# Kernel tuning notes

Measured on AMD Instinct MI355X. Metric: run time of the kernel, lower is better.

The kernel has to match this reference:

```python
import jax, jax.numpy as jnp
import numpy as np


def setup_inputs() -> dict:
    key = jax.random.key(0)
    ks = jax.random.split(key, 8)
    B, N, E_PER, M = 8, 50000, 1000000, 2048  # graphs, nodes/graph, edges/graph, decision neurons
    BN, E = B * N, B * E_PER
    x = jax.random.normal(ks[0], (BN, 1), dtype=jnp.float32)
    edge_weight = jax.random.uniform(ks[1], (E,), minval=0.0, maxval=10.0, dtype=jnp.float32)
    # within-graph edges with PyG-style batch offsets
    offs = jnp.repeat(jnp.arange(B, dtype=jnp.int32) * N, E_PER)
    src = jax.random.randint(ks[2], (E,), 0, N, dtype=jnp.int32) + offs
    dst = jax.random.randint(ks[3], (E,), 0, N, dtype=jnp.int32) + offs
    # indices where decision_making_vector == 1 (static for jit)
    dm_indices = jnp.sort(jax.random.randint(ks[4], (M,), 0, N, dtype=jnp.int32))
    fc_w = jax.random.normal(ks[5], (1, 1), dtype=jnp.float32)
    fc_b = jax.random.normal(ks[6], (1,), dtype=jnp.float32)
    return {"x": x, "edge_weight": edge_weight, "src": src, "dst": dst,
            "dm_indices": dm_indices, "fc_w": fc_w, "fc_b": fc_b,
            "batch_size": 8, "num_passes": 3}


def reference(x, edge_weight, src, dst, dm_indices, fc_w, fc_b, batch_size, num_passes):
    # log1p edge transform
    ew = jnp.log1p(edge_weight)  # [E]
    BN = x.shape[0]
    N = BN // batch_size
    h = x  # [BN, 1]
    # TrainableEdgeConv: num_passes rounds of scatter-add message passing + per-graph L2 norm over nodes
    for _ in range(num_passes):
        msgs = h[src] * ew[:, None]                      # [E, 1] gather + scale
        h = jax.ops.segment_sum(msgs, dst, num_segments=BN)  # scatter-add to dst
        hb = h.reshape(batch_size, N, -1)
        hb = hb / jnp.linalg.norm(hb, axis=1, keepdims=True)  # x / x.norm(dim=1)
        h = hb.reshape(BN, -1)
    # decision_making_mask: select decision neurons
    v = h.reshape(batch_size, N, -1)[:, dm_indices, 0]  # [B, M]
    # normalize_non_zero: per-graph mean/std over nonzero entries (unbiased std, like scatter_std)
    mask = v != 0
    cnt = mask.sum(axis=1, keepdims=True).astype(v.dtype)
    mean = jnp.where(mask, v, 0.0).sum(axis=1, keepdims=True) / cnt
    var = jnp.where(mask, (v - mean) ** 2, 0.0).sum(axis=1, keepdims=True) / jnp.maximum(cnt - 1.0, 1.0)
    std = jnp.sqrt(var) + 1e-5
    v = jnp.where(mask, (v - mean) / std, v)
    # mean pool over decision neurons, Linear(1,1), relu, squeeze -> [B]
    pooled = v.mean(axis=1)  # [B]
    out = pooled * fc_w[0, 0] + fc_b[0]
    return jax.nn.relu(out)
```

## Files before the change

### kernel.cpp

```cpp
#include <hip/hip_runtime.h>
#include <math.h>

#define GB    8
#define GN    50000
#define EPG   1000000
#define EDGES (GB*EPG)
#define NP    3

#define BW     4096
#define NBUCK  13
#define NBINS  (GB*NBUCK)
#define CAP    89088
#define CPB    10
#define STRIPE 4000
#define NQ     (STRIPE/4)
#define NBLKH  (EDGES/STRIPE)
#define BPG    (EPG/STRIPE)
#define SRCMASK 0x7FFFFu


__global__ void z_k(int* __restrict__ gcur, float* __restrict__ nsq) {
  int t = threadIdx.x;
  if (t < NBINS) gcur[t] = 0;
  if (t < GB) nsq[t] = 0.f;
}

__global__ __launch_bounds__(256) void fscatter_k(
    const int* __restrict__ src, const int* __restrict__ dst,
    const float* __restrict__ ew, int* __restrict__ gcur,
    uint2* __restrict__ recs) {
  __shared__ int lh[NBINS];
  __shared__ int lb[NBINS];
  if (threadIdx.x < NBINS) lh[threadIdx.x] = 0;
  __syncthreads();
  int blk = blockIdx.x;
  int s0 = blk * STRIPE;
  int g = blk / BPG;
  int base = g * GN, gb = g * NBUCK;
  const int4* d4 = (const int4*)(dst + s0);
  const int4* s4 = (const int4*)(src + s0);
  const float4* w4 = (const float4*)(ew + s0);

  int rk[16];
#pragma unroll
  for (int u = 0; u < 4; ++u) {
    int q = threadIdx.x + 256 * u;
    if (q < NQ) {
      int4 d = d4[q];
      rk[4 * u + 0] = atomicAdd(&lh[gb + ((d.x - base) >> 12)], 1);
      rk[4 * u + 1] = atomicAdd(&lh[gb + ((d.y - base) >> 12)], 1);
      rk[4 * u + 2] = atomicAdd(&lh[gb + ((d.z - base) >> 12)], 1);
      rk[4 * u + 3] = atomicAdd(&lh[gb + ((d.w - base) >> 12)], 1);
    }
  }
  __syncthreads();
  if (threadIdx.x < NBINS) {
    int c = lh[threadIdx.x];
    lb[threadIdx.x] = c ? atomicAdd(&gcur[threadIdx.x], c) : 0;
  }
  __syncthreads();
#pragma unroll
  for (int u = 0; u < 4; ++u) {
    int q = threadIdx.x + 256 * u;
    if (q < NQ) {
      int4 d = d4[q]; int4 s = s4[q]; float4 w = w4[q];
      int dv[4] = {d.x, d.y, d.z, d.w};
      int sv[4] = {s.x, s.y, s.z, s.w};
      float wv[4] = {w.x, w.y, w.z, w.w};
#pragma unroll
      for (int k = 0; k < 4; ++k) {
        int dl = dv[k] - base;
        int bin = gb + (dl >> 12);
        int r = dl & (BW - 1);
        size_t pos = (size_t)bin * CAP + lb[bin] + rk[4 * u + k];
        recs[pos] = make_uint2(((unsigned)r << 19) | (unsigned)sv[k],
                               __float_as_uint(log1pf(wv[k])));
      }
    }
  }
}

__global__ __launch_bounds__(256) void accum_k(
    const uint2* __restrict__ recs, const int* __restrict__ cnt,
    const float* __restrict__ hin, float* __restrict__ partials) {
  __shared__ float acc[BW];
  int c = blockIdx.x;
  int bin = blockIdx.y;
  float4 z = {0.f, 0.f, 0.f, 0.f};
  float4* a4 = (float4*)acc;
  for (int i = threadIdx.x; i < BW / 4; i += 256) a4[i] = z;
  int len = cnt[bin];
  int chunk = ((len + CPB - 1) / CPB + 1) & ~1;
  int lo = c * chunk;
  int hi = lo + chunk;
  if (lo > len) lo = len;
  if (hi > len) hi = len;
  const uint2* rb = recs + (size_t)bin * CAP;
  __syncthreads();
  int rem = hi - lo;
  if (rem < 0) rem = 0;
  int np = rem >> 1;
  const uint4* rp = (const uint4*)(rb + lo);
  int p = threadIdx.x;
  for (; p + 256 < np; p += 512) {
    uint4 r0 = rp[p];
    uint4 r1 = rp[p + 256];
    float a0 = hin[r0.x & SRCMASK] * __uint_as_float(r0.y);
    float a1 = hin[r0.z & SRCMASK] * __uint_as_float(r0.w);
    float a2 = hin[r1.x & SRCMASK] * __uint_as_float(r1.y);
    float a3 = hin[r1.z & SRCMASK] * __uint_as_float(r1.w);
    atomicAdd(&acc[r0.x >> 19], a0);
    atomicAdd(&acc[r0.z >> 19], a1);
    atomicAdd(&acc[r1.x >> 19], a2);
    atomicAdd(&acc[r1.z >> 19], a3);
  }
  if (p < np) {
    uint4 r0 = rp[p];
    atomicAdd(&acc[r0.x >> 19], hin[r0.x & SRCMASK] * __uint_as_float(r0.y));
    atomicAdd(&acc[r0.z >> 19], hin[r0.z & SRCMASK] * __uint_as_float(r0.w));
  }
  if ((rem & 1) && threadIdx.x == 0) {
    uint2 a = rb[hi - 1];
    atomicAdd(&acc[a.x >> 19], hin[a.x & SRCMASK] * __uint_as_float(a.y));
  }
  __syncthreads();
  float4* po = (float4*)(partials + ((size_t)bin * CPB + c) * BW);
  for (int i = threadIdx.x; i < BW / 4; i += 256) po[i] = a4[i];
}

__global__ void reduce_k(const float* __restrict__ partials,
                         float* __restrict__ hout, float* __restrict__ nsq) {
  __shared__ float sm[GB];
  if (threadIdx.x < GB) sm[threadIdx.x] = 0.f;
  __syncthreads();
  int n4 = blockIdx.x * 256 + threadIdx.x;
  if (n4 < (GB * GN) / 4) {
    int n = n4 * 4;
    int g = n / GN;
    int dl = n - g * GN;
    int bucket = dl >> 12;
    int slot = dl & (BW - 1);
    const float4* p = (const float4*)(partials +
        ((size_t)(g * NBUCK + bucket) * CPB) * BW + slot);
    float4 s = {0.f, 0.f, 0.f, 0.f};
#pragma unroll
    for (int c = 0; c < CPB; ++c) {
      float4 t = p[c * (BW / 4)];
      s.x += t.x; s.y += t.y; s.z += t.z; s.w += t.w;
    }
    ((float4*)hout)[n4] = s;
    if (nsq) atomicAdd(&sm[g], s.x * s.x + s.y * s.y + s.z * s.z + s.w * s.w);
  }
  __syncthreads();
  if (nsq && threadIdx.x < GB && sm[threadIdx.x] != 0.f)
    unsafeAtomicAdd(&nsq[threadIdx.x], sm[threadIdx.x]);
}


__global__ void init_k(const float* __restrict__ x, float* __restrict__ h_cur,
                       float* __restrict__ h_next, float* __restrict__ norms,
                       int BN, int n_norms) {
  int i = blockIdx.x * blockDim.x + threadIdx.x;
  int stride = gridDim.x * blockDim.x;
  for (int j = i; j < BN; j += stride) { h_cur[j] = x[j]; h_next[j] = 0.f; }
  if (i < n_norms) norms[i] = 0.f;
}

__global__ void edge_k(const int* __restrict__ src, const int* __restrict__ dst,
                       const float* __restrict__ ew, const float* __restrict__ h_in,
                       float* __restrict__ h_out, int E4, int E) {
  int i = blockIdx.x * blockDim.x + threadIdx.x;
  int stride = gridDim.x * blockDim.x;
  const int4* s4 = (const int4*)src;
  const int4* d4 = (const int4*)dst;
  const float4* w4 = (const float4*)ew;
  for (int j = i; j < E4; j += stride) {
    int4 s = s4[j]; int4 d = d4[j]; float4 w = w4[j];
    unsafeAtomicAdd(&h_out[d.x], h_in[s.x] * log1pf(w.x));
    unsafeAtomicAdd(&h_out[d.y], h_in[s.y] * log1pf(w.y));
    unsafeAtomicAdd(&h_out[d.z], h_in[s.z] * log1pf(w.z));
    unsafeAtomicAdd(&h_out[d.w], h_in[s.w] * log1pf(w.w));
  }
  for (int j = E4 * 4 + i; j < E; j += stride)
    unsafeAtomicAdd(&h_out[dst[j]], h_in[src[j]] * log1pf(ew[j]));
}

__global__ void norm_k(const float* __restrict__ h, float* __restrict__ norms, int N) {
  int g = blockIdx.y;
  const float* hg = h + (size_t)g * N;
  float s = 0.f;
  for (int j = blockIdx.x * blockDim.x + threadIdx.x; j < N; j += gridDim.x * blockDim.x) {
    float v = hg[j]; s += v * v;
  }
  __shared__ float sm[4];
  for (int o = 32; o > 0; o >>= 1) s += __shfl_down(s, o, 64);
  if ((threadIdx.x & 63) == 0) sm[threadIdx.x >> 6] = s;
  __syncthreads();
  if (threadIdx.x == 0) {
    float t = 0.f;
    for (int w = 0; w < (int)(blockDim.x >> 6); ++w) t += sm[w];
    unsafeAtomicAdd(&norms[g], t);
  }
}

__global__ void scale_k(const float* __restrict__ norms, float* __restrict__ h_next,
                        float* __restrict__ h_cur, int N) {
  int g = blockIdx.y;
  float inv = 1.0f / sqrtf(norms[g]);
  size_t off = (size_t)g * N;
  for (int j = blockIdx.x * blockDim.x + threadIdx.x; j < N; j += gridDim.x * blockDim.x) {
    h_cur[off + j] = h_next[off + j] * inv;
    h_next[off + j] = 0.f;
  }
}

__device__ __forceinline__ float blk_red(float t, float* sm, int nw) {
  for (int o = 32; o > 0; o >>= 1) t += __shfl_down(t, o, 64);
  if ((threadIdx.x & 63) == 0) sm[threadIdx.x >> 6] = t;
  __syncthreads();
  float r = 0.f;
  for (int w = 0; w < nw; ++w) r += sm[w];
  __syncthreads();
  return r;
}

__global__ void final_k(const float* __restrict__ h, const float* __restrict__ nsq,
                        const int* __restrict__ dm,
                        const float* __restrict__ fc_w, const float* __restrict__ fc_b,
                        float* __restrict__ out, int N, int M) {
  extern __shared__ float v[];
  __shared__ float sm[16];
  int b = blockIdx.x;
  int nw = blockDim.x >> 6;
  float inv = nsq ? 1.0f / sqrtf(nsq[b]) : 1.0f;
  const float* hb = h + (size_t)b * N;
  for (int m = threadIdx.x; m < M; m += blockDim.x) v[m] = hb[dm[m]] * inv;
  __syncthreads();

  float cnt = 0.f, sum = 0.f;
  for (int m = threadIdx.x; m < M; m += blockDim.x) {
    float xv = v[m];
    if (xv != 0.f) { cnt += 1.f; sum += xv; }
  }
  float totalSum = blk_red(sum, sm, nw);
  float totalCnt = blk_red(cnt, sm, nw);
  float mean = totalCnt > 0.f ? totalSum / totalCnt : 0.f;

  float ssq = 0.f;
  for (int m = threadIdx.x; m < M; m += blockDim.x) {
    float xv = v[m];
    if (xv != 0.f) { float d = xv - mean; ssq += d * d; }
  }
  float totalSsq = blk_red(ssq, sm, nw);

  float denom = totalCnt - 1.f;
  if (denom < 1.f) denom = 1.f;
  float stdv = sqrtf(totalSsq / denom) + 1e-5f;

  float ps = 0.f;
  for (int m = threadIdx.x; m < M; m += blockDim.x) {
    float xv = v[m];
    if (xv != 0.f) ps += (xv - mean) / stdv;
  }
  float pooled = blk_red(ps, sm, nw) / (float)M;
  if (threadIdx.x == 0) {
    float o = pooled * fc_w[0] + fc_b[0];
    out[b] = o > 0.f ? o : 0.f;
  }
}

extern "C" void kernel_launch(void* const* d_in, const int* in_sizes, int n_in,
                              void* d_out, int out_size, void* d_ws, size_t ws_size,
                              hipStream_t stream) {
  const float* x    = (const float*)d_in[0];
  const float* ew   = (const float*)d_in[1];
  const int*   src  = (const int*)d_in[2];
  const int*   dst  = (const int*)d_in[3];
  const int*   dm   = (const int*)d_in[4];
  const float* fc_w = (const float*)d_in[5];
  const float* fc_b = (const float*)d_in[6];

  const int BN = in_sizes[0];
  const int E  = in_sizes[1];
  const int M  = in_sizes[4];
  const int N  = BN / GB;

  const bool shapes_ok = (BN == GB * GN) && (E == EDGES);

  const size_t recs_b  = (size_t)NBINS * CAP * 8;
  const size_t part_b  = (size_t)NBINS * CPB * BW * 4;
  const size_t buf_b   = (size_t)BN * 4;
  const size_t misc_b  = 4096;
  const size_t REQ = recs_b + part_b + 2 * buf_b + misc_b;

  if (shapes_ok && ws_size >= REQ) {
    uint2* recs     = (uint2*)d_ws;
    float* partials = (float*)((char*)d_ws + recs_b);
    float* bufA     = (float*)((char*)partials + part_b);
    float* bufB     = (float*)((char*)bufA + buf_b);
    char*  misc     = (char*)bufB + buf_b;
    int*   gcur     = (int*)misc;
    float* nsq      = (float*)(gcur + NBINS + 8);

    z_k<<<1, 128, 0, stream>>>(gcur, nsq);
    fscatter_k<<<NBLKH, 256, 0, stream>>>(src, dst, ew, gcur, recs);

    int rgrid = (BN / 4 + 255) / 256;
    dim3 agrid(CPB, NBINS);
    accum_k<<<agrid, 256, 0, stream>>>(recs, gcur, x, partials);
    reduce_k<<<rgrid, 256, 0, stream>>>(partials, bufA, nullptr);
    accum_k<<<agrid, 256, 0, stream>>>(recs, gcur, bufA, partials);
    reduce_k<<<rgrid, 256, 0, stream>>>(partials, bufB, nullptr);
    accum_k<<<agrid, 256, 0, stream>>>(recs, gcur, bufB, partials);
    reduce_k<<<rgrid, 256, 0, stream>>>(partials, bufA, nsq);

    final_k<<<GB, 512, M * sizeof(float), stream>>>(bufA, nsq, dm, fc_w, fc_b,
                                                    (float*)d_out, N, M);
    return;
  }

  float* h_cur  = (float*)d_ws;
  float* h_next = h_cur + BN;
  float* norms  = h_next + BN;
  const int threads = 256;
  init_k<<<(BN + threads - 1) / threads, threads, 0, stream>>>(x, h_cur, h_next,
                                                               norms, BN, NP * GB);
  int E4 = E / 4;
  int edgeBlocks = (E4 + threads - 1) / threads;
  dim3 ngrid((N + threads * 8 - 1) / (threads * 8), GB);
  for (int p = 0; p < NP; ++p) {
    edge_k<<<edgeBlocks, threads, 0, stream>>>(src, dst, ew, h_cur, h_next, E4, E);
    norm_k<<<ngrid, threads, 0, stream>>>(h_next, norms + p * GB, N);
    scale_k<<<ngrid, threads, 0, stream>>>(norms + p * GB, h_next, h_cur, N);
  }
  final_k<<<GB, 256, M * sizeof(float), stream>>>(h_cur, nullptr, dm, fc_w, fc_b,
                                                  (float*)d_out, N, M);
}
```

Measured before the change: 334.6 us.

## Bin edges by source and destination bucket to stage h in LDS

Edges are now binned into a 2D grid of (source bucket, destination bucket) per graph, using an added counting pass and a prefix-scan so records are packed compactly rather than held in fixed-capacity bins. Each accumulation block loads its 4096-entry source slice of h into shared memory, which replaces random global gathers with LDS reads. The cost is an extra full read of src and dst in the count pass and a scan kernel. Blocks are now split by source bucket instead of fixed chunks, so per-block work is less even, and the reduce step sums 13 partials per destination instead of 10.

```diff
diff --git a/kernel.cpp b/kernel.cpp
--- a/kernel.cpp
+++ b/kernel.cpp
@@ -9,34 +9,93 @@
 
 #define BW     4096
 #define NBUCK  13
-#define NBINS  (GB*NBUCK)
-#define CAP    89088
-#define CPB    10
+#define LBINS  (NBUCK*NBUCK)
+#define NB2    (GB*LBINS)
 #define STRIPE 4000
 #define NQ     (STRIPE/4)
 #define NBLKH  (EDGES/STRIPE)
 #define BPG    (EPG/STRIPE)
-#define SRCMASK 0x7FFFFu
-
-
-__global__ void z_k(int* __restrict__ gcur, float* __restrict__ nsq) {
-  int t = threadIdx.x;
-  if (t < NBINS) gcur[t] = 0;
-  if (t < GB) nsq[t] = 0.f;
-}
-
-__global__ __launch_bounds__(256) void fscatter_k(
+#define SCHUNK 6
+
+
+__global__ void z_k(int* __restrict__ gcur, int* __restrict__ cnt,
+                    float* __restrict__ nsq) {
+  for (int i = threadIdx.x; i < NB2; i += 256) { gcur[i] = 0; cnt[i] = 0; }
+  if (threadIdx.x < GB) nsq[threadIdx.x] = 0.f;
+}
+
+__global__ __launch_bounds__(256) void count_k(
     const int* __restrict__ src, const int* __restrict__ dst,
-    const float* __restrict__ ew, int* __restrict__ gcur,
-    uint2* __restrict__ recs) {
-  __shared__ int lh[NBINS];
-  __shared__ int lb[NBINS];
-  if (threadIdx.x < NBINS) lh[threadIdx.x] = 0;
+    int* __restrict__ cnt) {
+  __shared__ int lh[LBINS];
+  for (int i = threadIdx.x; i < LBINS; i += 256) lh[i] = 0;
   __syncthreads();
   int blk = blockIdx.x;
   int s0 = blk * STRIPE;
   int g = blk / BPG;
-  int base = g * GN, gb = g * NBUCK;
+  int base = g * GN;
+  const int4* d4 = (const int4*)(dst + s0);
+  const int4* s4 = (const int4*)(src + s0);
+#pragma unroll
+  for (int u = 0; u < 4; ++u) {
+    int q = threadIdx.x + 256 * u;
+    if (q < NQ) {
+      int4 d = d4[q]; int4 s = s4[q];
+      atomicAdd(&lh[((s.x - base) >> 12) * NBUCK + ((d.x - base) >> 12)], 1);
+      atomicAdd(&lh[((s.y - base) >> 12) * NBUCK + ((d.y - base) >> 12)], 1);
+      atomicAdd(&lh[((s.z - base) >> 12) * NBUCK + ((d.z - base) >> 12)], 1);
+      atomicAdd(&lh[((s.w - base) >> 12) * NBUCK + ((d.w - base) >> 12)], 1);
+    }
+  }
+  __syncthreads();
+  int gb = g * LBINS;
+  for (int i = threadIdx.x; i < LBINS; i += 256) {
+    int c = lh[i];
+    if (c) atomicAdd(&cnt[gb + i], c);
+  }
+}
+
+__global__ void scan_k(const int* __restrict__ cnt, int* __restrict__ basea) {
+  __shared__ int ps[256];
+  int t = threadIdx.x;
+  int loc[SCHUNK];
+  int s = 0;
+#pragma unroll
+  for (int k = 0; k < SCHUNK; ++k) {
+    int i = t * SCHUNK + k;
+    int a = (i < NB2) ? ((cnt[i] + 1) & ~1) : 0;
+    loc[k] = s;
+    s += a;
+  }
+  ps[t] = s;
+  __syncthreads();
+  for (int o = 1; o < 256; o <<= 1) {
+    int u = (t >= o) ? ps[t - o] : 0;
+    __syncthreads();
+    ps[t] += u;
+    __syncthreads();
+  }
+  int ex = t ? ps[t - 1] : 0;
+#pragma unroll
+  for (int k = 0; k < SCHUNK; ++k) {
+    int i = t * SCHUNK + k;
+    if (i < NB2) basea[i] = ex + loc[k];
+  }
+  if (t == 255) basea[NB2] = ps[255];
+}
+
+__global__ __launch_bounds__(256) void fscatter_k(
+    const int* __restrict__ src, const int* __restrict__ dst,
+    const float* __restrict__ ew, const int* __restrict__ basea,
+    int* __restrict__ gcur, uint2* __restrict__ recs) {
+  __shared__ int lh[LBINS];
+  __shared__ int lb[LBINS];
+  for (int i = threadIdx.x; i < LBINS; i += 256) lh[i] = 0;
+  __syncthreads();
+  int blk = blockIdx.x;
+  int s0 = blk * STRIPE;
+  int g = blk / BPG;
+  int base = g * GN, gb = g * LBINS;
   const int4* d4 = (const int4*)(dst + s0);
   const int4* s4 = (const int4*)(src + s0);
   const float4* w4 = (const float4*)(ew + s0);
@@ -46,17 +105,17 @@
   for (int u = 0; u < 4; ++u) {
     int q = threadIdx.x + 256 * u;
     if (q < NQ) {
-      int4 d = d4[q];
-      rk[4 * u + 0] = atomicAdd(&lh[gb + ((d.x - base) >> 12)], 1);
-      rk[4 * u + 1] = atomicAdd(&lh[gb + ((d.y - base) >> 12)], 1);
-      rk[4 * u + 2] = atomicAdd(&lh[gb + ((d.z - base) >> 12)], 1);
-      rk[4 * u + 3] = atomicAdd(&lh[gb + ((d.w - base) >> 12)], 1);
+      int4 d = d4[q]; int4 s = s4[q];
+      rk[4 * u + 0] = atomicAdd(&lh[((s.x - base) >> 12) * NBUCK + ((d.x - base) >> 12)], 1);
+      rk[4 * u + 1] = atomicAdd(&lh[((s.y - base) >> 12) * NBUCK + ((d.y - base) >> 12)], 1);
+      rk[4 * u + 2] = atomicAdd(&lh[((s.z - base) >> 12) * NBUCK + ((d.z - base) >> 12)], 1);
+      rk[4 * u + 3] = atomicAdd(&lh[((s.w - base) >> 12) * NBUCK + ((d.w - base) >> 12)], 1);
     }
   }
   __syncthreads();
-  if (threadIdx.x < NBINS) {
-    int c = lh[threadIdx.x];
-    lb[threadIdx.x] = c ? atomicAdd(&gcur[threadIdx.x], c) : 0;
+  for (int i = threadIdx.x; i < LBINS; i += 256) {
+    int c = lh[i];
+    lb[i] = (c ? atomicAdd(&gcur[gb + i], c) : 0) + basea[gb + i];
   }
   __syncthreads();
 #pragma unroll
@@ -70,10 +129,11 @@
 #pragma unroll
       for (int k = 0; k < 4; ++k) {
         int dl = dv[k] - base;
-        int bin = gb + (dl >> 12);
-        int r = dl & (BW - 1);
-        size_t pos = (size_t)bin * CAP + lb[bin] + rk[4 * u + k];
-        recs[pos] = make_uint2(((unsigned)r << 19) | (unsigned)sv[k],
+        int sl = sv[k] - base;
+        int l = (sl >> 12) * NBUCK + (dl >> 12);
+        int pos = lb[l] + rk[4 * u + k];
+        recs[pos] = make_uint2(((unsigned)(dl & (BW - 1)) << 12) |
+                               (unsigned)(sl & (BW - 1)),
                                __float_as_uint(log1pf(wv[k])));
       }
     }
@@ -81,50 +141,54 @@
 }
 
 __global__ __launch_bounds__(256) void accum_k(
-    const uint2* __restrict__ recs, const int* __restrict__ cnt,
-    const float* __restrict__ hin, float* __restrict__ partials) {
+    const uint2* __restrict__ recs, const int* __restrict__ basea,
+    const int* __restrict__ cnt, const float* __restrict__ hin,
+    float* __restrict__ partials) {
+  __shared__ float sh[BW];
   __shared__ float acc[BW];
-  int c = blockIdx.x;
-  int bin = blockIdx.y;
+  int sb = blockIdx.x;
+  int gdb = blockIdx.y;
+  int g = gdb / NBUCK, db = gdb - g * NBUCK;
+  int bin = g * LBINS + sb * NBUCK + db;
+
   float4 z = {0.f, 0.f, 0.f, 0.f};
   float4* a4 = (float4*)acc;
   for (int i = threadIdx.x; i < BW / 4; i += 256) a4[i] = z;
+  int sw = GN - sb * BW; if (sw > BW) sw = BW;
+  const float4* hp = (const float4*)(hin + (size_t)g * GN + (size_t)sb * BW);
+  float4* sp = (float4*)sh;
+  for (int i = threadIdx.x; i < sw / 4; i += 256) sp[i] = hp[i];
+
   int len = cnt[bin];
-  int chunk = ((len + CPB - 1) / CPB + 1) & ~1;
-  int lo = c * chunk;
-  int hi = lo + chunk;
-  if (lo > len) lo = len;
-  if (hi > len) hi = len;
-  const uint2* rb = recs + (size_t)bin * CAP;
-  __syncthreads();
-  int rem = hi - lo;
-  if (rem < 0) rem = 0;
-  int np = rem >> 1;
-  const uint4* rp = (const uint4*)(rb + lo);
+  const uint2* rb = recs + basea[bin];
+  __syncthreads();
+
+  int np = len >> 1;
+  const uint4* rp = (const uint4*)rb;
   int p = threadIdx.x;
   for (; p + 256 < np; p += 512) {
     uint4 r0 = rp[p];
     uint4 r1 = rp[p + 256];
-    float a0 = hin[r0.x & SRCMASK] * __uint_as_float(r0.y);
-    float a1 = hin[r0.z & SRCMASK] * __uint_as_float(r0.w);
-    float a2 = hin[r1.x & SRCMASK] * __uint_as_float(r1.y);
-    float a3 = hin[r1.z & SRCMASK] * __uint_as_float(r1.w);
-    atomicAdd(&acc[r0.x >> 19], a0);
-    atomicAdd(&acc[r0.z >> 19], a1);
-    atomicAdd(&acc[r1.x >> 19], a2);
-    atomicAdd(&acc[r1.z >> 19], a3);
+    float a0 = sh[r0.x & (BW - 1)] * __uint_as_float(r0.y);
+    float a1 = sh[r0.z & (BW - 1)] * __uint_as_float(r0.w);
+    float a2 = sh[r1.x & (BW - 1)] * __uint_as_float(r1.y);
+    float a3 = sh[r1.z & (BW - 1)] * __uint_as_float(r1.w);
+    atomicAdd(&acc[r0.x >> 12], a0);
+    atomicAdd(&acc[r0.z >> 12], a1);
+    atomicAdd(&acc[r1.x >> 12], a2);
+    atomicAdd(&acc[r1.z >> 12], a3);
   }
   if (p < np) {
     uint4 r0 = rp[p];
-    atomicAdd(&acc[r0.x >> 19], hin[r0.x & SRCMASK] * __uint_as_float(r0.y));
-    atomicAdd(&acc[r0.z >> 19], hin[r0.z & SRCMASK] * __uint_as_float(r0.w));
-  }
-  if ((rem & 1) && threadIdx.x == 0) {
-    uint2 a = rb[hi - 1];
-    atomicAdd(&acc[a.x >> 19], hin[a.x & SRCMASK] * __uint_as_float(a.y));
-  }
-  __syncthreads();
-  float4* po = (float4*)(partials + ((size_t)bin * CPB + c) * BW);
+    atomicAdd(&acc[r0.x >> 12], sh[r0.x & (BW - 1)] * __uint_as_float(r0.y));
+    atomicAdd(&acc[r0.z >> 12], sh[r0.z & (BW - 1)] * __uint_as_float(r0.w));
+  }
+  if ((len & 1) && threadIdx.x == 0) {
+    uint2 a = rb[len - 1];
+    atomicAdd(&acc[a.x >> 12], sh[a.x & (BW - 1)] * __uint_as_float(a.y));
+  }
+  __syncthreads();
+  float4* po = (float4*)(partials + ((size_t)gdb * NBUCK + sb) * BW);
   for (int i = threadIdx.x; i < BW / 4; i += 256) po[i] = a4[i];
 }
 
@@ -141,10 +205,10 @@
     int bucket = dl >> 12;
     int slot = dl & (BW - 1);
     const float4* p = (const float4*)(partials +
-        ((size_t)(g * NBUCK + bucket) * CPB) * BW + slot);
+        ((size_t)(g * NBUCK + bucket) * NBUCK) * BW + slot);
     float4 s = {0.f, 0.f, 0.f, 0.f};
 #pragma unroll
-    for (int c = 0; c < CPB; ++c) {
+    for (int c = 0; c < NBUCK; ++c) {
       float4 t = p[c * (BW / 4)];
       s.x += t.x; s.y += t.y; s.z += t.z; s.w += t.w;
     }
@@ -287,10 +351,10 @@
 
   const bool shapes_ok = (BN == GB * GN) && (E == EDGES);
 
-  const size_t recs_b  = (size_t)NBINS * CAP * 8;
-  const size_t part_b  = (size_t)NBINS * CPB * BW * 4;
-  const size_t buf_b   = (size_t)BN * 4;
-  const size_t misc_b  = 4096;
+  const size_t recs_b = (size_t)(EDGES + 4096) * 8;
+  const size_t part_b = (size_t)GB * NBUCK * NBUCK * BW * 4;
+  const size_t buf_b  = (size_t)BN * 4;
+  const size_t misc_b = 65536;
   const size_t REQ = recs_b + part_b + 2 * buf_b + misc_b;
 
   if (shapes_ok && ws_size >= REQ) {
@@ -300,18 +364,22 @@
     float* bufB     = (float*)((char*)bufA + buf_b);
     char*  misc     = (char*)bufB + buf_b;
     int*   gcur     = (int*)misc;
-    float* nsq      = (float*)(gcur + NBINS + 8);
-
-    z_k<<<1, 128, 0, stream>>>(gcur, nsq);
-    fscatter_k<<<NBLKH, 256, 0, stream>>>(src, dst, ew, gcur, recs);
+    int*   cntp     = gcur + NB2;
+    int*   basea    = cntp + NB2;
+    float* nsq      = (float*)(basea + NB2 + 8);
+
+    z_k<<<1, 256, 0, stream>>>(gcur, cntp, nsq);
+    count_k<<<NBLKH, 256, 0, stream>>>(src, dst, cntp);
+    scan_k<<<1, 256, 0, stream>>>(cntp, basea);
+    fscatter_k<<<NBLKH, 256, 0, stream>>>(src, dst, ew, basea, gcur, recs);
 
     int rgrid = (BN / 4 + 255) / 256;
-    dim3 agrid(CPB, NBINS);
-    accum_k<<<agrid, 256, 0, stream>>>(recs, gcur, x, partials);
+    dim3 agrid(NBUCK, GB * NBUCK);
+    accum_k<<<agrid, 256, 0, stream>>>(recs, basea, cntp, x, partials);
     reduce_k<<<rgrid, 256, 0, stream>>>(partials, bufA, nullptr);
-    accum_k<<<agrid, 256, 0, stream>>>(recs, gcur, bufA, partials);
+    accum_k<<<agrid, 256, 0, stream>>>(recs, basea, cntp, bufA, partials);
     reduce_k<<<rgrid, 256, 0, stream>>>(partials, bufB, nullptr);
-    accum_k<<<agrid, 256, 0, stream>>>(recs, gcur, bufB, partials);
+    accum_k<<<agrid, 256, 0, stream>>>(recs, basea, cntp, bufB, partials);
     reduce_k<<<rgrid, 256, 0, stream>>>(partials, bufA, nsq);
 
     final_k<<<GB, 512, M * sizeof(float), stream>>>(bufA, nsq, dm, fc_w, fc_b,
```

Result: slower. 441.3 us (+31.9%).

## Drop partials/reduce kernels via global atomics and stage scatter records in LDS

Applied to the files above, without the earlier changes.

accum_k now adds its shared-memory accumulator straight into the global output buffer with atomics, skipping nonzero values. This removes the per-chunk partials buffer and all three reduce_k launches. The final-pass L2 norm moves into final_k, which recomputes the sum of squares from the output. fscatter_k now counting-sorts each smaller stripe into LDS before writing to the global bins, so the global writes are contiguous runs, at the cost of extra shared memory and a second pass.

```diff
diff --git a/kernel.cpp b/kernel.cpp
--- a/kernel.cpp
+++ b/kernel.cpp
@@ -12,26 +12,30 @@
 #define NBINS  (GB*NBUCK)
 #define CAP    89088
 #define CPB    10
-#define STRIPE 4000
+#define STRIPE 2000
 #define NQ     (STRIPE/4)
 #define NBLKH  (EDGES/STRIPE)
 #define BPG    (EPG/STRIPE)
 #define SRCMASK 0x7FFFFu
 
 
-__global__ void z_k(int* __restrict__ gcur, float* __restrict__ nsq) {
-  int t = threadIdx.x;
-  if (t < NBINS) gcur[t] = 0;
-  if (t < GB) nsq[t] = 0.f;
+__global__ void z_k(int* __restrict__ gcur, float4* __restrict__ a,
+                    float4* __restrict__ b, float4* __restrict__ c) {
+  int i = blockIdx.x * 256 + threadIdx.x;
+  float4 z = {0.f, 0.f, 0.f, 0.f};
+  if (i < (GB * GN) / 4) { a[i] = z; b[i] = z; c[i] = z; }
+  if (blockIdx.x == 0 && threadIdx.x < NBINS) gcur[threadIdx.x] = 0;
 }
 
 __global__ __launch_bounds__(256) void fscatter_k(
     const int* __restrict__ src, const int* __restrict__ dst,
     const float* __restrict__ ew, int* __restrict__ gcur,
     uint2* __restrict__ recs) {
-  __shared__ int lh[NBINS];
-  __shared__ int lb[NBINS];
-  if (threadIdx.x < NBINS) lh[threadIdx.x] = 0;
+  __shared__ int lh[NBUCK];
+  __shared__ int lsb[NBUCK];
+  __shared__ int lbg[NBUCK];
+  __shared__ uint2 srt[STRIPE];
+  if (threadIdx.x < NBUCK) lh[threadIdx.x] = 0;
   __syncthreads();
   int blk = blockIdx.x;
   int s0 = blk * STRIPE;
@@ -41,26 +45,29 @@
   const int4* s4 = (const int4*)(src + s0);
   const float4* w4 = (const float4*)(ew + s0);
 
-  int rk[16];
+  int rk[8];
 #pragma unroll
-  for (int u = 0; u < 4; ++u) {
+  for (int u = 0; u < 2; ++u) {
     int q = threadIdx.x + 256 * u;
     if (q < NQ) {
       int4 d = d4[q];
-      rk[4 * u + 0] = atomicAdd(&lh[gb + ((d.x - base) >> 12)], 1);
-      rk[4 * u + 1] = atomicAdd(&lh[gb + ((d.y - base) >> 12)], 1);
-      rk[4 * u + 2] = atomicAdd(&lh[gb + ((d.z - base) >> 12)], 1);
-      rk[4 * u + 3] = atomicAdd(&lh[gb + ((d.w - base) >> 12)], 1);
+      rk[4 * u + 0] = atomicAdd(&lh[(d.x - base) >> 12], 1);
+      rk[4 * u + 1] = atomicAdd(&lh[(d.y - base) >> 12], 1);
+      rk[4 * u + 2] = atomicAdd(&lh[(d.z - base) >> 12], 1);
+      rk[4 * u + 3] = atomicAdd(&lh[(d.w - base) >> 12], 1);
     }
   }
   __syncthreads();
-  if (threadIdx.x < NBINS) {
+  if (threadIdx.x < NBUCK) {
     int c = lh[threadIdx.x];
-    lb[threadIdx.x] = c ? atomicAdd(&gcur[threadIdx.x], c) : 0;
+    lbg[threadIdx.x] = c ? atomicAdd(&gcur[gb + threadIdx.x], c) : 0;
+    int s = 0;
+    for (int j = 0; j < threadIdx.x; ++j) s += lh[j];
+    lsb[threadIdx.x] = s;
   }
   __syncthreads();
 #pragma unroll
-  for (int u = 0; u < 4; ++u) {
+  for (int u = 0; u < 2; ++u) {
     int q = threadIdx.x + 256 * u;
     if (q < NQ) {
       int4 d = d4[q]; int4 s = s4[q]; float4 w = w4[q];
@@ -70,19 +77,25 @@
 #pragma unroll
       for (int k = 0; k < 4; ++k) {
         int dl = dv[k] - base;
-        int bin = gb + (dl >> 12);
-        int r = dl & (BW - 1);
-        size_t pos = (size_t)bin * CAP + lb[bin] + rk[4 * u + k];
-        recs[pos] = make_uint2(((unsigned)r << 19) | (unsigned)sv[k],
-                               __float_as_uint(log1pf(wv[k])));
+        int bin = dl >> 12;
+        srt[lsb[bin] + rk[4 * u + k]] =
+            make_uint2(((unsigned)(dl & (BW - 1)) << 19) | (unsigned)sv[k],
+                       __float_as_uint(log1pf(wv[k])));
       }
     }
   }
+  __syncthreads();
+  for (int b = 0; b < NBUCK; ++b) {
+    int cnt = lh[b];
+    int lo = lsb[b];
+    uint2* dp = recs + (size_t)(gb + b) * CAP + lbg[b];
+    for (int i = threadIdx.x; i < cnt; i += 256) dp[i] = srt[lo + i];
+  }
 }
 
 __global__ __launch_bounds__(256) void accum_k(
     const uint2* __restrict__ recs, const int* __restrict__ cnt,
-    const float* __restrict__ hin, float* __restrict__ partials) {
+    const float* __restrict__ hin, float* __restrict__ hout) {
   __shared__ float acc[BW];
   int c = blockIdx.x;
   int bin = blockIdx.y;
@@ -124,36 +137,13 @@
     atomicAdd(&acc[a.x >> 19], hin[a.x & SRCMASK] * __uint_as_float(a.y));
   }
   __syncthreads();
-  float4* po = (float4*)(partials + ((size_t)bin * CPB + c) * BW);
-  for (int i = threadIdx.x; i < BW / 4; i += 256) po[i] = a4[i];
-}
-
-__global__ void reduce_k(const float* __restrict__ partials,
-                         float* __restrict__ hout, float* __restrict__ nsq) {
-  __shared__ float sm[GB];
-  if (threadIdx.x < GB) sm[threadIdx.x] = 0.f;
-  __syncthreads();
-  int n4 = blockIdx.x * 256 + threadIdx.x;
-  if (n4 < (GB * GN) / 4) {
-    int n = n4 * 4;
-    int g = n / GN;
-    int dl = n - g * GN;
-    int bucket = dl >> 12;
-    int slot = dl & (BW - 1);
-    const float4* p = (const float4*)(partials +
-        ((size_t)(g * NBUCK + bucket) * CPB) * BW + slot);
-    float4 s = {0.f, 0.f, 0.f, 0.f};
-#pragma unroll
-    for (int c = 0; c < CPB; ++c) {
-      float4 t = p[c * (BW / 4)];
-      s.x += t.x; s.y += t.y; s.z += t.z; s.w += t.w;
-    }
-    ((float4*)hout)[n4] = s;
-    if (nsq) atomicAdd(&sm[g], s.x * s.x + s.y * s.y + s.z * s.z + s.w * s.w);
-  }
-  __syncthreads();
-  if (nsq && threadIdx.x < GB && sm[threadIdx.x] != 0.f)
-    unsafeAtomicAdd(&nsq[threadIdx.x], sm[threadIdx.x]);
+  int g = bin / NBUCK, bucket = bin - g * NBUCK;
+  int sw = GN - bucket * BW; if (sw > BW) sw = BW;
+  float* ho = hout + (size_t)g * GN + (size_t)bucket * BW;
+  for (int i = threadIdx.x; i < sw; i += 256) {
+    float v = acc[i];
+    if (v != 0.f) unsafeAtomicAdd(&ho[i], v);
+  }
 }
 
 
@@ -224,16 +214,27 @@
   return r;
 }
 
-__global__ void final_k(const float* __restrict__ h, const float* __restrict__ nsq,
-                        const int* __restrict__ dm,
+__global__ void final_k(const float* __restrict__ h, const int* __restrict__ dm,
                         const float* __restrict__ fc_w, const float* __restrict__ fc_b,
-                        float* __restrict__ out, int N, int M) {
+                        float* __restrict__ out, int N, int M, int do_norm) {
   extern __shared__ float v[];
   __shared__ float sm[16];
   int b = blockIdx.x;
   int nw = blockDim.x >> 6;
-  float inv = nsq ? 1.0f / sqrtf(nsq[b]) : 1.0f;
   const float* hb = h + (size_t)b * N;
+  float inv = 1.0f;
+  if (do_norm) {
+    const float4* h4 = (const float4*)hb;
+    float s = 0.f;
+    for (int i = threadIdx.x; i < N / 4; i += blockDim.x) {
+      float4 t = h4[i];
+      s += t.x * t.x + t.y * t.y + t.z * t.z + t.w * t.w;
+    }
+    for (int i = N & ~3; i < N; ++i)
+      if (threadIdx.x == 0) s += hb[i] * hb[i];
+    float tot = blk_red(s, sm, nw);
+    inv = 1.0f / sqrtf(tot);
+  }
   for (int m = threadIdx.x; m < M; m += blockDim.x) v[m] = hb[dm[m]] * inv;
   __syncthreads();
 
@@ -287,35 +288,29 @@
 
   const bool shapes_ok = (BN == GB * GN) && (E == EDGES);
 
-  const size_t recs_b  = (size_t)NBINS * CAP * 8;
-  const size_t part_b  = (size_t)NBINS * CPB * BW * 4;
-  const size_t buf_b   = (size_t)BN * 4;
-  const size_t misc_b  = 4096;
-  const size_t REQ = recs_b + part_b + 2 * buf_b + misc_b;
+  const size_t recs_b = (size_t)NBINS * CAP * 8;
+  const size_t buf_b  = (size_t)BN * 4;
+  const size_t misc_b = 4096;
+  const size_t REQ = recs_b + 3 * buf_b + misc_b;
 
   if (shapes_ok && ws_size >= REQ) {
-    uint2* recs     = (uint2*)d_ws;
-    float* partials = (float*)((char*)d_ws + recs_b);
-    float* bufA     = (float*)((char*)partials + part_b);
-    float* bufB     = (float*)((char*)bufA + buf_b);
-    char*  misc     = (char*)bufB + buf_b;
-    int*   gcur     = (int*)misc;
-    float* nsq      = (float*)(gcur + NBINS + 8);
-
-    z_k<<<1, 128, 0, stream>>>(gcur, nsq);
+    uint2* recs = (uint2*)d_ws;
+    float* bufA = (float*)((char*)d_ws + recs_b);
+    float* bufB = bufA + BN;
+    float* bufC = bufB + BN;
+    int*   gcur = (int*)(bufC + BN);
+
+    z_k<<<(BN / 4 + 255) / 256, 256, 0, stream>>>(gcur, (float4*)bufA,
+                                                  (float4*)bufB, (float4*)bufC);
     fscatter_k<<<NBLKH, 256, 0, stream>>>(src, dst, ew, gcur, recs);
 
-    int rgrid = (BN / 4 + 255) / 256;
     dim3 agrid(CPB, NBINS);
-    accum_k<<<agrid, 256, 0, stream>>>(recs, gcur, x, partials);
-    reduce_k<<<rgrid, 256, 0, stream>>>(partials, bufA, nullptr);
-    accum_k<<<agrid, 256, 0, stream>>>(recs, gcur, bufA, partials);
-    reduce_k<<<rgrid, 256, 0, stream>>>(partials, bufB, nullptr);
-    accum_k<<<agrid, 256, 0, stream>>>(recs, gcur, bufB, partials);
-    reduce_k<<<rgrid, 256, 0, stream>>>(partials, bufA, nsq);
-
-    final_k<<<GB, 512, M * sizeof(float), stream>>>(bufA, nsq, dm, fc_w, fc_b,
-                                                    (float*)d_out, N, M);
+    accum_k<<<agrid, 256, 0, stream>>>(recs, gcur, x, bufA);
+    accum_k<<<agrid, 256, 0, stream>>>(recs, gcur, bufA, bufB);
+    accum_k<<<agrid, 256, 0, stream>>>(recs, gcur, bufB, bufC);
+
+    final_k<<<GB, 512, M * sizeof(float), stream>>>(bufC, dm, fc_w, fc_b,
+                                                    (float*)d_out, N, M, 1);
     return;
   }
 
@@ -333,6 +328,6 @@
     norm_k<<<ngrid, threads, 0, stream>>>(h_next, norms + p * GB, N);
     scale_k<<<ngrid, threads, 0, stream>>>(norms + p * GB, h_next, h_cur, N);
   }
-  final_k<<<GB, 256, M * sizeof(float), stream>>>(h_cur, nullptr, dm, fc_w, fc_b,
-                                                  (float*)d_out, N, M);
-}
+  final_k<<<GB, 256, M * sizeof(float), stream>>>(h_cur, dm, fc_w, fc_b,
+                                                  (float*)d_out, N, M, 0);
+}
```

After: 339.2 us. Within noise of the previous version (+1.4%).

## Replace partials+reduce passes with direct global atomic flush and wider accum blocks

Applied to the files above, without the earlier changes.

Each accumulation block now flushes its shared-memory bucket straight into the output vector with global float atomics, so the per-pass partials buffer and the reduce kernel go away. Three output buffers are zeroed up front in the init kernel, and a separate small kernel computes the final squared norms. The accumulation kernel moves to 512 threads, with an 8-way batched load, gather and atomic loop for more memory-level parallelism. This trades the partials write and read traffic and two kernel launches for contended global atomics and a nondeterministic summation order.

```diff
diff --git a/kernel.cpp b/kernel.cpp
--- a/kernel.cpp
+++ b/kernel.cpp
@@ -19,10 +19,16 @@
 #define SRCMASK 0x7FFFFu
 
 
-__global__ void z_k(int* __restrict__ gcur, float* __restrict__ nsq) {
-  int t = threadIdx.x;
-  if (t < NBINS) gcur[t] = 0;
-  if (t < GB) nsq[t] = 0.f;
+__global__ void z_k(int* __restrict__ gcur, float* __restrict__ nsq,
+                    float4* __restrict__ a, float4* __restrict__ b,
+                    float4* __restrict__ c) {
+  int i = blockIdx.x * 256 + threadIdx.x;
+  float4 z = {0.f, 0.f, 0.f, 0.f};
+  if (i < (GB * GN) / 4) { a[i] = z; b[i] = z; c[i] = z; }
+  if (blockIdx.x == 0) {
+    if (threadIdx.x < NBINS) gcur[threadIdx.x] = 0;
+    if (threadIdx.x < GB) nsq[threadIdx.x] = 0.f;
+  }
 }
 
 __global__ __launch_bounds__(256) void fscatter_k(
@@ -80,15 +86,15 @@
   }
 }
 
-__global__ __launch_bounds__(256) void accum_k(
+__global__ __launch_bounds__(512) void accum_k(
     const uint2* __restrict__ recs, const int* __restrict__ cnt,
-    const float* __restrict__ hin, float* __restrict__ partials) {
+    const float* __restrict__ hin, float* __restrict__ hout) {
   __shared__ float acc[BW];
   int c = blockIdx.x;
   int bin = blockIdx.y;
   float4 z = {0.f, 0.f, 0.f, 0.f};
   float4* a4 = (float4*)acc;
-  for (int i = threadIdx.x; i < BW / 4; i += 256) a4[i] = z;
+  for (int i = threadIdx.x; i < BW / 4; i += 512) a4[i] = z;
   int len = cnt[bin];
   int chunk = ((len + CPB - 1) / CPB + 1) & ~1;
   int lo = c * chunk;
@@ -101,58 +107,57 @@
   if (rem < 0) rem = 0;
   int np = rem >> 1;
   const uint4* rp = (const uint4*)(rb + lo);
-  int p = threadIdx.x;
-  for (; p + 256 < np; p += 512) {
-    uint4 r0 = rp[p];
-    uint4 r1 = rp[p + 256];
-    float a0 = hin[r0.x & SRCMASK] * __uint_as_float(r0.y);
-    float a1 = hin[r0.z & SRCMASK] * __uint_as_float(r0.w);
-    float a2 = hin[r1.x & SRCMASK] * __uint_as_float(r1.y);
-    float a3 = hin[r1.z & SRCMASK] * __uint_as_float(r1.w);
-    atomicAdd(&acc[r0.x >> 19], a0);
-    atomicAdd(&acc[r0.z >> 19], a1);
-    atomicAdd(&acc[r1.x >> 19], a2);
-    atomicAdd(&acc[r1.z >> 19], a3);
-  }
-  if (p < np) {
-    uint4 r0 = rp[p];
-    atomicAdd(&acc[r0.x >> 19], hin[r0.x & SRCMASK] * __uint_as_float(r0.y));
-    atomicAdd(&acc[r0.z >> 19], hin[r0.z & SRCMASK] * __uint_as_float(r0.w));
+  for (int base = 0; base < np; base += 8 * 512) {
+    uint4 r[8];
+    float av[8][2];
+#pragma unroll
+    for (int k = 0; k < 8; ++k) {
+      int idx = base + threadIdx.x + k * 512;
+      if (idx < np) r[k] = rp[idx];
+    }
+#pragma unroll
+    for (int k = 0; k < 8; ++k) {
+      int idx = base + threadIdx.x + k * 512;
+      if (idx < np) {
+        av[k][0] = hin[r[k].x & SRCMASK] * __uint_as_float(r[k].y);
+        av[k][1] = hin[r[k].z & SRCMASK] * __uint_as_float(r[k].w);
+      }
+    }
+#pragma unroll
+    for (int k = 0; k < 8; ++k) {
+      int idx = base + threadIdx.x + k * 512;
+      if (idx < np) {
+        atomicAdd(&acc[r[k].x >> 19], av[k][0]);
+        atomicAdd(&acc[r[k].z >> 19], av[k][1]);
+      }
+    }
   }
   if ((rem & 1) && threadIdx.x == 0) {
     uint2 a = rb[hi - 1];
     atomicAdd(&acc[a.x >> 19], hin[a.x & SRCMASK] * __uint_as_float(a.y));
   }
   __syncthreads();
-  float4* po = (float4*)(partials + ((size_t)bin * CPB + c) * BW);
-  for (int i = threadIdx.x; i < BW / 4; i += 256) po[i] = a4[i];
-}
-
-__global__ void reduce_k(const float* __restrict__ partials,
-                         float* __restrict__ hout, float* __restrict__ nsq) {
+  int g = bin / NBUCK, bucket = bin - g * NBUCK;
+  int sw = GN - bucket * BW; if (sw > BW) sw = BW;
+  float* ho = hout + (size_t)g * GN + (size_t)bucket * BW;
+  for (int i = threadIdx.x; i < sw; i += 512) {
+    float v = acc[i];
+    if (v != 0.f) unsafeAtomicAdd(&ho[i], v);
+  }
+}
+
+__global__ void nsq_k(const float4* __restrict__ h4, float* __restrict__ nsq) {
   __shared__ float sm[GB];
   if (threadIdx.x < GB) sm[threadIdx.x] = 0.f;
   __syncthreads();
   int n4 = blockIdx.x * 256 + threadIdx.x;
   if (n4 < (GB * GN) / 4) {
-    int n = n4 * 4;
-    int g = n / GN;
-    int dl = n - g * GN;
-    int bucket = dl >> 12;
-    int slot = dl & (BW - 1);
-    const float4* p = (const float4*)(partials +
-        ((size_t)(g * NBUCK + bucket) * CPB) * BW + slot);
-    float4 s = {0.f, 0.f, 0.f, 0.f};
-#pragma unroll
-    for (int c = 0; c < CPB; ++c) {
-      float4 t = p[c * (BW / 4)];
-      s.x += t.x; s.y += t.y; s.z += t.z; s.w += t.w;
-    }
-    ((float4*)hout)[n4] = s;
-    if (nsq) atomicAdd(&sm[g], s.x * s.x + s.y * s.y + s.z * s.z + s.w * s.w);
-  }
-  __syncthreads();
-  if (nsq && threadIdx.x < GB && sm[threadIdx.x] != 0.f)
+    float4 t = h4[n4];
+    int g = (n4 * 4) / GN;
+    atomicAdd(&sm[g], t.x * t.x + t.y * t.y + t.z * t.z + t.w * t.w);
+  }
+  __syncthreads();
+  if (threadIdx.x < GB && sm[threadIdx.x] != 0.f)
     unsafeAtomicAdd(&nsq[threadIdx.x], sm[threadIdx.x]);
 }
 
@@ -287,34 +292,30 @@
 
   const bool shapes_ok = (BN == GB * GN) && (E == EDGES);
 
-  const size_t recs_b  = (size_t)NBINS * CAP * 8;
-  const size_t part_b  = (size_t)NBINS * CPB * BW * 4;
-  const size_t buf_b   = (size_t)BN * 4;
-  const size_t misc_b  = 4096;
-  const size_t REQ = recs_b + part_b + 2 * buf_b + misc_b;
+  const size_t recs_b = (size_t)NBINS * CAP * 8;
+  const size_t buf_b  = (size_t)BN * 4;
+  const size_t misc_b = 4096;
+  const size_t REQ = recs_b + 3 * buf_b + misc_b;
 
   if (shapes_ok && ws_size >= REQ) {
-    uint2* recs     = (uint2*)d_ws;
-    float* partials = (float*)((char*)d_ws + recs_b);
-    float* bufA     = (float*)((char*)partials + part_b);
-    float* bufB     = (float*)((char*)bufA + buf_b);
-    char*  misc     = (char*)bufB + buf_b;
-    int*   gcur     = (int*)misc;
-    float* nsq      = (float*)(gcur + NBINS + 8);
-
-    z_k<<<1, 128, 0, stream>>>(gcur, nsq);
+    uint2* recs = (uint2*)d_ws;
+    float* bufA = (float*)((char*)d_ws + recs_b);
+    float* bufB = bufA + BN;
+    float* bufC = bufB + BN;
+    int*   gcur = (int*)(bufC + BN);
+    float* nsq  = (float*)(gcur + NBINS + 8);
+
+    z_k<<<(BN / 4 + 255) / 256, 256, 0, stream>>>(gcur, nsq, (float4*)bufA,
+                                                  (float4*)bufB, (float4*)bufC);
     fscatter_k<<<NBLKH, 256, 0, stream>>>(src, dst, ew, gcur, recs);
 
-    int rgrid = (BN / 4 + 255) / 256;
     dim3 agrid(CPB, NBINS);
-    accum_k<<<agrid, 256, 0, stream>>>(recs, gcur, x, partials);
-    reduce_k<<<rgrid, 256, 0, stream>>>(partials, bufA, nullptr);
-    accum_k<<<agrid, 256, 0, stream>>>(recs, gcur, bufA, partials);
-    reduce_k<<<rgrid, 256, 0, stream>>>(partials, bufB, nullptr);
-    accum_k<<<agrid, 256, 0, stream>>>(recs, gcur, bufB, partials);
-    reduce_k<<<rgrid, 256, 0, stream>>>(partials, bufA, nsq);
-
-    final_k<<<GB, 512, M * sizeof(float), stream>>>(bufA, nsq, dm, fc_w, fc_b,
+    accum_k<<<agrid, 512, 0, stream>>>(recs, gcur, x, bufA);
+    accum_k<<<agrid, 512, 0, stream>>>(recs, gcur, bufA, bufB);
+    accum_k<<<agrid, 512, 0, stream>>>(recs, gcur, bufB, bufC);
+
+    nsq_k<<<(BN / 4 + 255) / 256, 256, 0, stream>>>((const float4*)bufC, nsq);
+    final_k<<<GB, 512, M * sizeof(float), stream>>>(bufC, nsq, dm, fc_w, fc_b,
                                                     (float*)d_out, N, M);
     return;
   }
```

Result: slower. 407.6 us (+21.8%).
